# Optimization experiments

Hardware: AMD Instinct MI355X
Metric: run time of the kernel (lower is better)

Reference implementation:

```python
import jax, jax.numpy as jnp
import numpy as np

B, T, C = 16, 4096, 64  # batch, seq_len, n_embd == head_size


def setup_inputs() -> dict:
    key = jax.random.key(0)
    k1, k2, k3, k4 = jax.random.split(key, 4)
    x = jax.random.normal(k1, (B, T, C), dtype=jnp.float32)
    Wq = jax.random.normal(k2, (C, C), dtype=jnp.float32) * (C ** -0.5)
    Wk = jax.random.normal(k3, (C, C), dtype=jnp.float32) * (C ** -0.5)
    Wv = jax.random.normal(k4, (C, C), dtype=jnp.float32) * (C ** -0.5)
    return {"x": x, "Wq": Wq, "Wk": Wk, "Wv": Wv}


def reference(x, Wq, Wk, Wv):
    # Single-head causal self-attention (dropout rate = 0.0 in source -> identity).
    q = jnp.einsum('btc,cd->btd', x, Wq)  # [B,T,D]
    k = jnp.einsum('btc,cd->btd', x, Wk)  # [B,T,D]
    v = jnp.einsum('btc,cd->btd', x, Wv)  # [B,T,D]
    scale = q.shape[-1] ** -0.5
    wei = jnp.einsum('btd,bsd->bts', q, k) * scale  # [B,T,T] scores
    causal = jnp.tril(jnp.ones((T, T), dtype=bool))  # [T,T]
    wei = jnp.where(causal[None, :, :], wei, jnp.finfo(wei.dtype).min)
    wei = jax.nn.softmax(wei, axis=-1)
    out = jnp.einsum('bts,bsd->btd', wei, v)  # [B,T,D]
    return out
```

## Files before the change

kernel.cpp:

```cpp
#include <hip/hip_runtime.h>
#include <hip/hip_bf16.h>
#include <math.h>

#define BATCH 16
#define SEQ 4096
#define HDIM 64

typedef __attribute__((ext_vector_type(8))) short bf16x8;
typedef __attribute__((ext_vector_type(4))) float f32x4;
typedef __attribute__((ext_vector_type(4))) unsigned int u32x4;
typedef __attribute__((ext_vector_type(8))) unsigned short us8;

#define QSCALE 0.1803368801111601f

static __device__ __forceinline__ float exp2_fast(float x) {
#if __has_builtin(__builtin_amdgcn_exp2f)
    return __builtin_amdgcn_exp2f(x);
#else
    float r; asm("v_exp_f32 %0, %1" : "=v"(r) : "v"(x)); return r;
#endif
}

static __device__ __forceinline__ void load_lds16(const void* g, void* l) {
    __builtin_amdgcn_global_load_lds(
        (const __attribute__((address_space(1))) unsigned int*)g,
        (__attribute__((address_space(3))) unsigned int*)l,
        16, 0, 0);
}

static __device__ __forceinline__ unsigned short bf16bits(float f) {
    __hip_bfloat16 h = __float2bfloat16(f);
    return *(unsigned short*)&h;
}

static __device__ __forceinline__ unsigned int pack_bf16_trunc(float f0, float f1) {
    unsigned int u0 = __builtin_bit_cast(unsigned int, f0);
    unsigned int u1 = __builtin_bit_cast(unsigned int, f1);
#if __has_builtin(__builtin_amdgcn_perm)
    return __builtin_amdgcn_perm(u1, u0, 0x07060302u);
#else
    return (u1 & 0xFFFF0000u) | (u0 >> 16);
#endif
}

__global__ __launch_bounds__(256)
void wconv_kernel(const float* __restrict__ Wq,
                  const float* __restrict__ Wk,
                  const float* __restrict__ Wv,
                  __hip_bfloat16* __restrict__ wsw) {
    const int mat = blockIdx.x;
    const int tid = threadIdx.x;
    const float* W = (mat == 0) ? Wq : (mat == 1) ? Wk : Wv;
    const float sc = (mat == 0) ? QSCALE : 1.0f;
    #pragma unroll
    for (int c2 = 0; c2 < 2; ++c2) {
        const int chunk = c2 * 256 + tid;
        const int n = chunk & 63;
        const int c = chunk >> 6;
        us8 u;
        #pragma unroll
        for (int j = 0; j < 8; ++j)
            u[j] = bf16bits(W[(c * 8 + j) * HDIM + n] * sc);
        *(us8*)(wsw + mat * 4096 + n * 64 + (size_t)(c ^ (n & 7)) * 8) = u;
    }
}

__global__ __launch_bounds__(256)
void qkv_mfma_kernel(const float* __restrict__ x,
                     const __hip_bfloat16* __restrict__ wsw,
                     __hip_bfloat16* __restrict__ qb,
                     __hip_bfloat16* __restrict__ kb,
                     __hip_bfloat16* __restrict__ vt) {
    __shared__ __attribute__((aligned(16))) __hip_bfloat16 swt[3 * 64 * 64];
    __shared__ __attribute__((aligned(16))) char spool[16384];
    float* sx = (float*)spool;
    __hip_bfloat16 (*sout)[80] = (__hip_bfloat16 (*)[80])spool;

    const int tid = threadIdx.x;
    const int wv = tid >> 6;
    const int lane = tid & 63;
    const int quad = lane >> 4;
    const int ml = lane & 15;
    const size_t row0 = (size_t)blockIdx.x * 64;
    const int batch = (int)(row0 >> 12);
    const int t0 = (int)(row0 & 4095);

    #pragma unroll
    for (int r = 0; r < 6; ++r)
        load_lds16(wsw + (size_t)(r * 256 + tid) * 8, swt + (size_t)(r * 256 + tid) * 8);
    #pragma unroll
    for (int r = 0; r < 4; ++r)
        load_lds16(x + row0 * HDIM + (size_t)(r * 256 + tid) * 4, sx + (size_t)(r * 256 + tid) * 4);
    asm volatile("s_waitcnt vmcnt(0)" ::: "memory");
    __syncthreads();

    bf16x8 a0, a1;
    {
        const float* xr = sx + (size_t)(wv * 16 + ml) * HDIM + quad * 8;
        f32x4 lo = *(const f32x4*)xr;
        f32x4 hi = *(const f32x4*)(xr + 4);
        u32x4 pk;
        pk[0] = pack_bf16_trunc(lo[0], lo[1]);
        pk[1] = pack_bf16_trunc(lo[2], lo[3]);
        pk[2] = pack_bf16_trunc(hi[0], hi[1]);
        pk[3] = pack_bf16_trunc(hi[2], hi[3]);
        a0 = __builtin_bit_cast(bf16x8, pk);
        lo = *(const f32x4*)(xr + 32);
        hi = *(const f32x4*)(xr + 36);
        pk[0] = pack_bf16_trunc(lo[0], lo[1]);
        pk[1] = pack_bf16_trunc(lo[2], lo[3]);
        pk[2] = pack_bf16_trunc(hi[0], hi[1]);
        pk[3] = pack_bf16_trunc(hi[2], hi[3]);
        a1 = __builtin_bit_cast(bf16x8, pk);
    }
    __syncthreads();

    #pragma unroll
    for (int mat = 0; mat < 3; ++mat) {
        const __hip_bfloat16* wb = swt + mat * 4096;
        f32x4 acc[4];
        #pragma unroll
        for (int nt = 0; nt < 4; ++nt) {
            const int n = nt * 16 + ml;
            const int nx = n & 7;
            const bf16x8 bl = *(const bf16x8*)(wb + (size_t)n * 64 + (size_t)((quad) ^ nx) * 8);
            const bf16x8 bh = *(const bf16x8*)(wb + (size_t)n * 64 + (size_t)((quad + 4) ^ nx) * 8);
            acc[nt] = __builtin_amdgcn_mfma_f32_16x16x32_bf16(a0, bl, (f32x4){0.f,0.f,0.f,0.f}, 0, 0, 0);
            acc[nt] = __builtin_amdgcn_mfma_f32_16x16x32_bf16(a1, bh, acc[nt], 0, 0, 0);
        }

        if (mat < 2) {
            #pragma unroll
            for (int nt = 0; nt < 4; ++nt)
                #pragma unroll
                for (int r = 0; r < 4; ++r)
                    sout[wv * 16 + quad * 4 + r][nt * 16 + ml] = __float2bfloat16(acc[nt][r]);
        } else {
            #pragma unroll
            for (int nt = 0; nt < 4; ++nt)
                #pragma unroll
                for (int r = 0; r < 4; ++r)
                    sout[nt * 16 + ml][(wv >> 1) * 32 + quad * 8 + (wv & 1) * 4 + r] =
                        __float2bfloat16(acc[nt][r]);
        }
        __syncthreads();
        __hip_bfloat16* dst = (mat == 0) ? qb : (mat == 1) ? kb : vt;
        #pragma unroll
        for (int c2 = 0; c2 < 2; ++c2) {
            const int cc = c2 * 256 + tid;
            const int row = cc >> 3, g = cc & 7;
            us8 u = *(const us8*)&sout[row][g * 8];
            if (mat < 2)
                *(us8*)(dst + (row0 + row) * HDIM + g * 8) = u;
            else
                *(us8*)(dst + ((size_t)batch * HDIM + row) * SEQ + t0 + g * 8) = u;
        }
        __syncthreads();
    }
}

__global__ __launch_bounds__(256, 4)
void flash_mfma_kernel(const __hip_bfloat16* __restrict__ qb,
                       const __hip_bfloat16* __restrict__ kbuf,
                       const __hip_bfloat16* __restrict__ vt,
                       float* __restrict__ out) {
    __shared__ __attribute__((aligned(16))) __hip_bfloat16 smem[16384];

    const int tid = threadIdx.x;
    const int wv = tid >> 6;
    const int lane = tid & 63;
    const int quad = lane >> 4;
    const int ml = lane & 15;
    const int mh = wv & 1;
    const int kh = wv >> 1;

    const int id = blockIdx.x;
    const int b = id & 15;
    const int t = id >> 4;
    const int hi2 = t >> 4, mid = t & 15;
    const int qt = (hi2 == 0) ? (63 - mid)
                 : (hi2 == 1) ? (32 + mid)
                 : (hi2 == 2) ? (31 - mid) : mid;
    const int qbw = qt * 64 + mh * 32;
    const size_t bb = (size_t)b * SEQ * HDIM;

    const __hip_bfloat16* Q = qb + bb;
    const __hip_bfloat16* K = kbuf + bb;
    const __hip_bfloat16* VT = vt + bb;

    bf16x8 bq[2][2];
    #pragma unroll
    for (int qi = 0; qi < 2; ++qi)
        #pragma unroll
        for (int h = 0; h < 2; ++h)
            bq[qi][h] = *(const bf16x8*)(Q + (size_t)(qbw + qi * 16 + ml) * HDIM + h * 32 + quad * 8);

    bf16x8 ones8;
    #pragma unroll
    for (int j = 0; j < 8; ++j) ones8[j] = (short)0x3F80;

    f32x4 acc[4][2];
    #pragma unroll
    for (int nt = 0; nt < 4; ++nt)
        #pragma unroll
        for (int qi = 0; qi < 2; ++qi) acc[nt][qi] = (f32x4){0.f, 0.f, 0.f, 0.f};
    f32x4 lacc[2] = {(f32x4){0.f,0.f,0.f,0.f}, (f32x4){0.f,0.f,0.f,0.f}};

    const int s0 = wv * 128 + lane;
    const int s1 = s0 + 64;
    const int r0row = s0 >> 3, r0ch = (s0 & 7) ^ (r0row & 7);
    const int r1row = s1 >> 3, r1ch = (s1 & 7) ^ (r1row & 7);
    const int d0 = (wv * 128) * 8;
    const int d1 = (wv * 128 + 64) * 8;

    int koff[2][2], voff[4];
    #pragma unroll
    for (int kt = 0; kt < 2; ++kt) {
        const int row = kh * 32 + kt * 16 + ml;
        const int rb = row << 3, rxx = row & 7;
        koff[kt][0] = (rb | (quad ^ rxx)) * 8;
        koff[kt][1] = (rb | ((quad + 4) ^ rxx)) * 8;
    }
    #pragma unroll
    for (int nt = 0; nt < 4; ++nt) {
        const int row = nt * 16 + ml;
        const int rb = row << 3, rxx = row & 7;
        voff[nt] = (rb | ((kh * 4 + quad) ^ rxx)) * 8;
    }

    load_lds16(K + (size_t)r0row * HDIM + r0ch * 8, smem + d0);
    load_lds16(K + (size_t)r1row * HDIM + r1ch * 8, smem + d1);
    load_lds16(VT + (size_t)r0row * SEQ + r0ch * 8, smem + 8192 + d0);
    load_lds16(VT + (size_t)r1row * SEQ + r1ch * 8, smem + 8192 + d1);
    asm volatile("s_waitcnt vmcnt(0)" ::: "memory");
    __syncthreads();

    for (int tile = 0; tile < qt; ++tile) {
        const int sel = (tile & 1) * 4096;
        const int nsel = 4096 - sel;
        const __hip_bfloat16* sk = smem + sel;
        const __hip_bfloat16* sv = smem + 8192 + sel;

        const int nk = tile * 64 + 64;
        load_lds16(K + (size_t)(nk + r0row) * HDIM + r0ch * 8, smem + nsel + d0);
        load_lds16(K + (size_t)(nk + r1row) * HDIM + r1ch * 8, smem + nsel + d1);
        load_lds16(VT + (size_t)r0row * SEQ + nk + r0ch * 8, smem + 8192 + nsel + d0);
        load_lds16(VT + (size_t)r1row * SEQ + nk + r1ch * 8, smem + 8192 + nsel + d1);

        bf16x8 kf[2][2], va[4];
        #pragma unroll
        for (int kt = 0; kt < 2; ++kt) {
            kf[kt][0] = *(const bf16x8*)(sk + koff[kt][0]);
            kf[kt][1] = *(const bf16x8*)(sk + koff[kt][1]);
        }
        #pragma unroll
        for (int nt = 0; nt < 4; ++nt)
            va[nt] = *(const bf16x8*)(sv + voff[nt]);

        f32x4 st[2][2];
        __builtin_amdgcn_s_setprio(1);
        #pragma unroll
        for (int kt = 0; kt < 2; ++kt)
            #pragma unroll
            for (int qi = 0; qi < 2; ++qi) {
                st[kt][qi] = __builtin_amdgcn_mfma_f32_16x16x32_bf16(kf[kt][0], bq[qi][0], (f32x4){0.f,0.f,0.f,0.f}, 0, 0, 0);
                st[kt][qi] = __builtin_amdgcn_mfma_f32_16x16x32_bf16(kf[kt][1], bq[qi][1], st[kt][qi], 0, 0, 0);
            }
        __builtin_amdgcn_s_setprio(0);

        bf16x8 p80;
        {
            float pv[8];
            #pragma unroll
            for (int half = 0; half < 2; ++half)
                #pragma unroll
                for (int r = 0; r < 4; ++r)
                    pv[half * 4 + r] = exp2_fast(st[half][0][r]);
            u32x4 pk;
            #pragma unroll
            for (int d = 0; d < 4; ++d)
                pk[d] = pack_bf16_trunc(pv[2 * d], pv[2 * d + 1]);
            p80 = __builtin_bit_cast(bf16x8, pk);
        }

        __builtin_amdgcn_s_setprio(1);
        lacc[0] = __builtin_amdgcn_mfma_f32_16x16x32_bf16(ones8, p80, lacc[0], 0, 0, 0);
        #pragma unroll
        for (int nt = 0; nt < 4; ++nt)
            acc[nt][0] = __builtin_amdgcn_mfma_f32_16x16x32_bf16(va[nt], p80, acc[nt][0], 0, 0, 0);
        __builtin_amdgcn_s_setprio(0);

        bf16x8 p81;
        {
            float pv[8];
            #pragma unroll
            for (int half = 0; half < 2; ++half)
                #pragma unroll
                for (int r = 0; r < 4; ++r)
                    pv[half * 4 + r] = exp2_fast(st[half][1][r]);
            u32x4 pk;
            #pragma unroll
            for (int d = 0; d < 4; ++d)
                pk[d] = pack_bf16_trunc(pv[2 * d], pv[2 * d + 1]);
            p81 = __builtin_bit_cast(bf16x8, pk);
        }

        __builtin_amdgcn_s_setprio(1);
        lacc[1] = __builtin_amdgcn_mfma_f32_16x16x32_bf16(ones8, p81, lacc[1], 0, 0, 0);
        #pragma unroll
        for (int nt = 0; nt < 4; ++nt)
            acc[nt][1] = __builtin_amdgcn_mfma_f32_16x16x32_bf16(va[nt], p81, acc[nt][1], 0, 0, 0);
        __builtin_amdgcn_s_setprio(0);

        asm volatile("s_waitcnt vmcnt(0)" ::: "memory");
        __syncthreads();
    }

    {
        const int kb0 = qt * 64;
        const int sel = (qt & 1) * 4096;
        const __hip_bfloat16* sk = smem + sel;
        const __hip_bfloat16* sv = smem + 8192 + sel;

        if (!(kh == 1 && mh == 0)) {
            bf16x8 kf[2][2], va[4];
            #pragma unroll
            for (int kt = 0; kt < 2; ++kt) {
                kf[kt][0] = *(const bf16x8*)(sk + koff[kt][0]);
                kf[kt][1] = *(const bf16x8*)(sk + koff[kt][1]);
            }
            #pragma unroll
            for (int nt = 0; nt < 4; ++nt)
                va[nt] = *(const bf16x8*)(sv + voff[nt]);

            f32x4 st[2][2];
            #pragma unroll
            for (int kt = 0; kt < 2; ++kt)
                #pragma unroll
                for (int qi = 0; qi < 2; ++qi) {
                    st[kt][qi] = __builtin_amdgcn_mfma_f32_16x16x32_bf16(kf[kt][0], bq[qi][0], (f32x4){0.f,0.f,0.f,0.f}, 0, 0, 0);
                    st[kt][qi] = __builtin_amdgcn_mfma_f32_16x16x32_bf16(kf[kt][1], bq[qi][1], st[kt][qi], 0, 0, 0);
                }

            bf16x8 p8[2];
            #pragma unroll
            for (int qi = 0; qi < 2; ++qi) {
                const int q = qbw + qi * 16 + ml;
                float pv[8];
                #pragma unroll
                for (int half = 0; half < 2; ++half)
                    #pragma unroll
                    for (int r = 0; r < 4; ++r) {
                        const int key = kb0 + kh * 32 + half * 16 + quad * 4 + r;
                        float pval = exp2_fast(st[half][qi][r]);
                        if (key > q) pval = 0.f;
                        pv[half * 4 + r] = pval;
                    }
                u32x4 pk;
                #pragma unroll
                for (int d = 0; d < 4; ++d)
                    pk[d] = pack_bf16_trunc(pv[2 * d], pv[2 * d + 1]);
                p8[qi] = __builtin_bit_cast(bf16x8, pk);
            }

            lacc[0] = __builtin_amdgcn_mfma_f32_16x16x32_bf16(ones8, p8[0], lacc[0], 0, 0, 0);
            lacc[1] = __builtin_amdgcn_mfma_f32_16x16x32_bf16(ones8, p8[1], lacc[1], 0, 0, 0);
            #pragma unroll
            for (int nt = 0; nt < 4; ++nt) {
                acc[nt][0] = __builtin_amdgcn_mfma_f32_16x16x32_bf16(va[nt], p8[0], acc[nt][0], 0, 0, 0);
                acc[nt][1] = __builtin_amdgcn_mfma_f32_16x16x32_bf16(va[nt], p8[1], acc[nt][1], 0, 0, 0);
            }
        }
    }

    float (*smerge)[64][18] = (float (*)[64][18])smem;
    #pragma unroll
    for (int qi = 0; qi < 2; ++qi) {
        __syncthreads();
        if (kh == 1) {
            float* mrow = smerge[mh][lane];
            #pragma unroll
            for (int nt = 0; nt < 4; ++nt)
                #pragma unroll
                for (int r = 0; r < 4; ++r) mrow[nt * 4 + r] = acc[nt][qi][r];
            mrow[16] = lacc[qi][0];
        }
        __syncthreads();
        if (kh == 0) {
            const float* mrow = smerge[mh][lane];
            const float inv = 1.0f / (lacc[qi][0] + mrow[16]);
            float* orow = out + bb + (size_t)(qbw + qi * 16 + ml) * HDIM;
            #pragma unroll
            for (int nt = 0; nt < 4; ++nt) {
                float4 o;
                o.x = (acc[nt][qi][0] + mrow[nt * 4 + 0]) * inv;
                o.y = (acc[nt][qi][1] + mrow[nt * 4 + 1]) * inv;
                o.z = (acc[nt][qi][2] + mrow[nt * 4 + 2]) * inv;
                o.w = (acc[nt][qi][3] + mrow[nt * 4 + 3]) * inv;
                *(float4*)(orow + nt * 16 + quad * 4) = o;
            }
        }
    }
}

extern "C" void kernel_launch(void* const* d_in, const int* in_sizes, int n_in,
                              void* d_out, int out_size, void* d_ws, size_t ws_size,
                              hipStream_t stream) {
    const float* x  = (const float*)d_in[0];
    const float* Wq = (const float*)d_in[1];
    const float* Wk = (const float*)d_in[2];
    const float* Wv = (const float*)d_in[3];
    float* outp = (float*)d_out;

    const size_t elems = (size_t)BATCH * SEQ * HDIM;
    __hip_bfloat16* qb = (__hip_bfloat16*)d_ws;
    __hip_bfloat16* kb = qb + elems;
    __hip_bfloat16* vt = kb + elems;
    __hip_bfloat16* wsw = vt + elems;

    wconv_kernel<<<dim3(3), 256, 0, stream>>>(Wq, Wk, Wv, wsw);
    qkv_mfma_kernel<<<dim3(BATCH * SEQ / 64), 256, 0, stream>>>(x, wsw, qb, kb, vt);
    flash_mfma_kernel<<<dim3(BATCH * SEQ / 64), 256, 0, stream>>>(qb, kb, vt, outp);
}
```

Baseline: 118.7 us.

## Split flash attention work across eight waves with one query subtile each

The flash attention kernel now launches 512 threads per block. Each wave owns a single 16-row query subtile instead of two, which halves per-wave accumulator registers and doubles waves per block. K/V tile loads are spread over eight waves at one load each, and the final cross-key-half merge runs once instead of per subtile. The QKV projection also swaps its packed truncation for a per-element bf16 conversion, which may change rounding and instruction count. The cost is more waves sharing each LDS tile, duplicated K/V fragment reads per wave, and higher barrier cost.

```diff
diff --git a/kernel.cpp b/kernel.cpp
--- a/kernel.cpp
+++ b/kernel.cpp
@@ -97,21 +97,10 @@
     bf16x8 a0, a1;
     {
         const float* xr = sx + (size_t)(wv * 16 + ml) * HDIM + quad * 8;
-        f32x4 lo = *(const f32x4*)xr;
-        f32x4 hi = *(const f32x4*)(xr + 4);
-        u32x4 pk;
-        pk[0] = pack_bf16_trunc(lo[0], lo[1]);
-        pk[1] = pack_bf16_trunc(lo[2], lo[3]);
-        pk[2] = pack_bf16_trunc(hi[0], hi[1]);
-        pk[3] = pack_bf16_trunc(hi[2], hi[3]);
-        a0 = __builtin_bit_cast(bf16x8, pk);
-        lo = *(const f32x4*)(xr + 32);
-        hi = *(const f32x4*)(xr + 36);
-        pk[0] = pack_bf16_trunc(lo[0], lo[1]);
-        pk[1] = pack_bf16_trunc(lo[2], lo[3]);
-        pk[2] = pack_bf16_trunc(hi[0], hi[1]);
-        pk[3] = pack_bf16_trunc(hi[2], hi[3]);
-        a1 = __builtin_bit_cast(bf16x8, pk);
+        #pragma unroll
+        for (int j = 0; j < 8; ++j) a0[j] = (short)bf16bits(xr[j]);
+        #pragma unroll
+        for (int j = 0; j < 8; ++j) a1[j] = (short)bf16bits(xr[32 + j]);
     }
     __syncthreads();
 
@@ -159,7 +148,7 @@
     }
 }
 
-__global__ __launch_bounds__(256, 4)
+__global__ __launch_bounds__(512, 8)
 void flash_mfma_kernel(const __hip_bfloat16* __restrict__ qb,
                        const __hip_bfloat16* __restrict__ kbuf,
                        const __hip_bfloat16* __restrict__ vt,
@@ -171,8 +160,9 @@
     const int lane = tid & 63;
     const int quad = lane >> 4;
     const int ml = lane & 15;
-    const int mh = wv & 1;
-    const int kh = wv >> 1;
+    const int kh = wv >> 2;
+    const int mh = (wv >> 1) & 1;
+    const int qj = wv & 1;
 
     const int id = blockIdx.x;
     const int b = id & 15;
@@ -181,37 +171,31 @@
     const int qt = (hi2 == 0) ? (63 - mid)
                  : (hi2 == 1) ? (32 + mid)
                  : (hi2 == 2) ? (31 - mid) : mid;
-    const int qbw = qt * 64 + mh * 32;
+    const int qbase = qt * 64 + mh * 32 + qj * 16;
     const size_t bb = (size_t)b * SEQ * HDIM;
 
     const __hip_bfloat16* Q = qb + bb;
     const __hip_bfloat16* K = kbuf + bb;
     const __hip_bfloat16* VT = vt + bb;
 
-    bf16x8 bq[2][2];
-    #pragma unroll
-    for (int qi = 0; qi < 2; ++qi)
-        #pragma unroll
-        for (int h = 0; h < 2; ++h)
-            bq[qi][h] = *(const bf16x8*)(Q + (size_t)(qbw + qi * 16 + ml) * HDIM + h * 32 + quad * 8);
+    bf16x8 bq[2];
+    #pragma unroll
+    for (int h = 0; h < 2; ++h)
+        bq[h] = *(const bf16x8*)(Q + (size_t)(qbase + ml) * HDIM + h * 32 + quad * 8);
 
     bf16x8 ones8;
     #pragma unroll
     for (int j = 0; j < 8; ++j) ones8[j] = (short)0x3F80;
 
-    f32x4 acc[4][2];
-    #pragma unroll
-    for (int nt = 0; nt < 4; ++nt)
-        #pragma unroll
-        for (int qi = 0; qi < 2; ++qi) acc[nt][qi] = (f32x4){0.f, 0.f, 0.f, 0.f};
-    f32x4 lacc[2] = {(f32x4){0.f,0.f,0.f,0.f}, (f32x4){0.f,0.f,0.f,0.f}};
-
-    const int s0 = wv * 128 + lane;
-    const int s1 = s0 + 64;
-    const int r0row = s0 >> 3, r0ch = (s0 & 7) ^ (r0row & 7);
-    const int r1row = s1 >> 3, r1ch = (s1 & 7) ^ (r1row & 7);
-    const int d0 = (wv * 128) * 8;
-    const int d1 = (wv * 128 + 64) * 8;
+    f32x4 acc[4];
+    #pragma unroll
+    for (int nt = 0; nt < 4; ++nt) acc[nt] = (f32x4){0.f, 0.f, 0.f, 0.f};
+    f32x4 lacc = (f32x4){0.f, 0.f, 0.f, 0.f};
+
+    const int kr = tid >> 3;
+    const int kc = (tid & 7) ^ (kr & 7);
+    __hip_bfloat16* const kds = smem + wv * 512;
+    __hip_bfloat16* const vds = smem + 8192 + wv * 512;
 
     int koff[2][2], voff[4];
     #pragma unroll
@@ -228,10 +212,8 @@
         voff[nt] = (rb | ((kh * 4 + quad) ^ rxx)) * 8;
     }
 
-    load_lds16(K + (size_t)r0row * HDIM + r0ch * 8, smem + d0);
-    load_lds16(K + (size_t)r1row * HDIM + r1ch * 8, smem + d1);
-    load_lds16(VT + (size_t)r0row * SEQ + r0ch * 8, smem + 8192 + d0);
-    load_lds16(VT + (size_t)r1row * SEQ + r1ch * 8, smem + 8192 + d1);
+    load_lds16(K + (size_t)kr * HDIM + kc * 8, kds);
+    load_lds16(VT + (size_t)kr * SEQ + kc * 8, vds);
     asm volatile("s_waitcnt vmcnt(0)" ::: "memory");
     __syncthreads();
 
@@ -242,74 +224,50 @@
         const __hip_bfloat16* sv = smem + 8192 + sel;
 
         const int nk = tile * 64 + 64;
-        load_lds16(K + (size_t)(nk + r0row) * HDIM + r0ch * 8, smem + nsel + d0);
-        load_lds16(K + (size_t)(nk + r1row) * HDIM + r1ch * 8, smem + nsel + d1);
-        load_lds16(VT + (size_t)r0row * SEQ + nk + r0ch * 8, smem + 8192 + nsel + d0);
-        load_lds16(VT + (size_t)r1row * SEQ + nk + r1ch * 8, smem + 8192 + nsel + d1);
-
-        bf16x8 kf[2][2], va[4];
+        load_lds16(K + (size_t)(nk + kr) * HDIM + kc * 8, smem + nsel + wv * 512);
+        load_lds16(VT + (size_t)kr * SEQ + nk + kc * 8, smem + 8192 + nsel + wv * 512);
+
+        bf16x8 kf[2][2];
         #pragma unroll
         for (int kt = 0; kt < 2; ++kt) {
             kf[kt][0] = *(const bf16x8*)(sk + koff[kt][0]);
             kf[kt][1] = *(const bf16x8*)(sk + koff[kt][1]);
         }
+
+        f32x4 st[2];
+        __builtin_amdgcn_s_setprio(1);
+        #pragma unroll
+        for (int kt = 0; kt < 2; ++kt) {
+            st[kt] = __builtin_amdgcn_mfma_f32_16x16x32_bf16(kf[kt][0], bq[0], (f32x4){0.f,0.f,0.f,0.f}, 0, 0, 0);
+            st[kt] = __builtin_amdgcn_mfma_f32_16x16x32_bf16(kf[kt][1], bq[1], st[kt], 0, 0, 0);
+        }
+        __builtin_amdgcn_s_setprio(0);
+
+        bf16x8 va[4];
         #pragma unroll
         for (int nt = 0; nt < 4; ++nt)
             va[nt] = *(const bf16x8*)(sv + voff[nt]);
 
-        f32x4 st[2][2];
-        __builtin_amdgcn_s_setprio(1);
-        #pragma unroll
-        for (int kt = 0; kt < 2; ++kt)
-            #pragma unroll
-            for (int qi = 0; qi < 2; ++qi) {
-                st[kt][qi] = __builtin_amdgcn_mfma_f32_16x16x32_bf16(kf[kt][0], bq[qi][0], (f32x4){0.f,0.f,0.f,0.f}, 0, 0, 0);
-                st[kt][qi] = __builtin_amdgcn_mfma_f32_16x16x32_bf16(kf[kt][1], bq[qi][1], st[kt][qi], 0, 0, 0);
-            }
-        __builtin_amdgcn_s_setprio(0);
-
-        bf16x8 p80;
+        bf16x8 p8;
         {
             float pv[8];
             #pragma unroll
-            for (int half = 0; half < 2; ++half)
+            for (int kt = 0; kt < 2; ++kt)
                 #pragma unroll
                 for (int r = 0; r < 4; ++r)
-                    pv[half * 4 + r] = exp2_fast(st[half][0][r]);
+                    pv[kt * 4 + r] = exp2_fast(st[kt][r]);
             u32x4 pk;
             #pragma unroll
             for (int d = 0; d < 4; ++d)
                 pk[d] = pack_bf16_trunc(pv[2 * d], pv[2 * d + 1]);
-            p80 = __builtin_bit_cast(bf16x8, pk);
+            p8 = __builtin_bit_cast(bf16x8, pk);
         }
 
         __builtin_amdgcn_s_setprio(1);
-        lacc[0] = __builtin_amdgcn_mfma_f32_16x16x32_bf16(ones8, p80, lacc[0], 0, 0, 0);
+        lacc = __builtin_amdgcn_mfma_f32_16x16x32_bf16(ones8, p8, lacc, 0, 0, 0);
         #pragma unroll
         for (int nt = 0; nt < 4; ++nt)
-            acc[nt][0] = __builtin_amdgcn_mfma_f32_16x16x32_bf16(va[nt], p80, acc[nt][0], 0, 0, 0);
-        __builtin_amdgcn_s_setprio(0);
-
-        bf16x8 p81;
-        {
-            float pv[8];
-            #pragma unroll
-            for (int half = 0; half < 2; ++half)
-                #pragma unroll
-                for (int r = 0; r < 4; ++r)
-                    pv[half * 4 + r] = exp2_fast(st[half][1][r]);
-            u32x4 pk;
-            #pragma unroll
-            for (int d = 0; d < 4; ++d)
-                pk[d] = pack_bf16_trunc(pv[2 * d], pv[2 * d + 1]);
-            p81 = __builtin_bit_cast(bf16x8, pk);
-        }
-
-        __builtin_amdgcn_s_setprio(1);
-        lacc[1] = __builtin_amdgcn_mfma_f32_16x16x32_bf16(ones8, p81, lacc[1], 0, 0, 0);
-        #pragma unroll
-        for (int nt = 0; nt < 4; ++nt)
-            acc[nt][1] = __builtin_amdgcn_mfma_f32_16x16x32_bf16(va[nt], p81, acc[nt][1], 0, 0, 0);
+            acc[nt] = __builtin_amdgcn_mfma_f32_16x16x32_bf16(va[nt], p8, acc[nt], 0, 0, 0);
         __builtin_amdgcn_s_setprio(0);
 
         asm volatile("s_waitcnt vmcnt(0)" ::: "memory");
@@ -323,82 +281,74 @@
         const __hip_bfloat16* sv = smem + 8192 + sel;
 
         if (!(kh == 1 && mh == 0)) {
-            bf16x8 kf[2][2], va[4];
+            bf16x8 kf[2][2];
             #pragma unroll
             for (int kt = 0; kt < 2; ++kt) {
                 kf[kt][0] = *(const bf16x8*)(sk + koff[kt][0]);
                 kf[kt][1] = *(const bf16x8*)(sk + koff[kt][1]);
             }
+            f32x4 st[2];
+            #pragma unroll
+            for (int kt = 0; kt < 2; ++kt) {
+                st[kt] = __builtin_amdgcn_mfma_f32_16x16x32_bf16(kf[kt][0], bq[0], (f32x4){0.f,0.f,0.f,0.f}, 0, 0, 0);
+                st[kt] = __builtin_amdgcn_mfma_f32_16x16x32_bf16(kf[kt][1], bq[1], st[kt], 0, 0, 0);
+            }
+            bf16x8 va[4];
             #pragma unroll
             for (int nt = 0; nt < 4; ++nt)
                 va[nt] = *(const bf16x8*)(sv + voff[nt]);
 
-            f32x4 st[2][2];
-            #pragma unroll
-            for (int kt = 0; kt < 2; ++kt)
-                #pragma unroll
-                for (int qi = 0; qi < 2; ++qi) {
-                    st[kt][qi] = __builtin_amdgcn_mfma_f32_16x16x32_bf16(kf[kt][0], bq[qi][0], (f32x4){0.f,0.f,0.f,0.f}, 0, 0, 0);
-                    st[kt][qi] = __builtin_amdgcn_mfma_f32_16x16x32_bf16(kf[kt][1], bq[qi][1], st[kt][qi], 0, 0, 0);
-                }
-
-            bf16x8 p8[2];
-            #pragma unroll
-            for (int qi = 0; qi < 2; ++qi) {
-                const int q = qbw + qi * 16 + ml;
+            bf16x8 p8;
+            {
+                const int q = qbase + ml;
                 float pv[8];
                 #pragma unroll
-                for (int half = 0; half < 2; ++half)
+                for (int kt = 0; kt < 2; ++kt)
                     #pragma unroll
                     for (int r = 0; r < 4; ++r) {
-                        const int key = kb0 + kh * 32 + half * 16 + quad * 4 + r;
-                        float pval = exp2_fast(st[half][qi][r]);
+                        const int key = kb0 + kh * 32 + kt * 16 + quad * 4 + r;
+                        float pval = exp2_fast(st[kt][r]);
                         if (key > q) pval = 0.f;
-                        pv[half * 4 + r] = pval;
+                        pv[kt * 4 + r] = pval;
                     }
                 u32x4 pk;
                 #pragma unroll
                 for (int d = 0; d < 4; ++d)
                     pk[d] = pack_bf16_trunc(pv[2 * d], pv[2 * d + 1]);
-                p8[qi] = __builtin_bit_cast(bf16x8, pk);
+                p8 = __builtin_bit_cast(bf16x8, pk);
             }
 
-            lacc[0] = __builtin_amdgcn_mfma_f32_16x16x32_bf16(ones8, p8[0], lacc[0], 0, 0, 0);
-            lacc[1] = __builtin_amdgcn_mfma_f32_16x16x32_bf16(ones8, p8[1], lacc[1], 0, 0, 0);
-            #pragma unroll
-            for (int nt = 0; nt < 4; ++nt) {
-                acc[nt][0] = __builtin_amdgcn_mfma_f32_16x16x32_bf16(va[nt], p8[0], acc[nt][0], 0, 0, 0);
-                acc[nt][1] = __builtin_amdgcn_mfma_f32_16x16x32_bf16(va[nt], p8[1], acc[nt][1], 0, 0, 0);
-            }
+            lacc = __builtin_amdgcn_mfma_f32_16x16x32_bf16(ones8, p8, lacc, 0, 0, 0);
+            #pragma unroll
+            for (int nt = 0; nt < 4; ++nt)
+                acc[nt] = __builtin_amdgcn_mfma_f32_16x16x32_bf16(va[nt], p8, acc[nt], 0, 0, 0);
         }
     }
 
     float (*smerge)[64][18] = (float (*)[64][18])smem;
-    #pragma unroll
-    for (int qi = 0; qi < 2; ++qi) {
-        __syncthreads();
-        if (kh == 1) {
-            float* mrow = smerge[mh][lane];
-            #pragma unroll
-            for (int nt = 0; nt < 4; ++nt)
-                #pragma unroll
-                for (int r = 0; r < 4; ++r) mrow[nt * 4 + r] = acc[nt][qi][r];
-            mrow[16] = lacc[qi][0];
-        }
-        __syncthreads();
-        if (kh == 0) {
-            const float* mrow = smerge[mh][lane];
-            const float inv = 1.0f / (lacc[qi][0] + mrow[16]);
-            float* orow = out + bb + (size_t)(qbw + qi * 16 + ml) * HDIM;
-            #pragma unroll
-            for (int nt = 0; nt < 4; ++nt) {
-                float4 o;
-                o.x = (acc[nt][qi][0] + mrow[nt * 4 + 0]) * inv;
-                o.y = (acc[nt][qi][1] + mrow[nt * 4 + 1]) * inv;
-                o.z = (acc[nt][qi][2] + mrow[nt * 4 + 2]) * inv;
-                o.w = (acc[nt][qi][3] + mrow[nt * 4 + 3]) * inv;
-                *(float4*)(orow + nt * 16 + quad * 4) = o;
-            }
+    const int pid = wv & 3;
+    __syncthreads();
+    if (kh == 1) {
+        float* mrow = smerge[pid][lane];
+        #pragma unroll
+        for (int nt = 0; nt < 4; ++nt)
+            #pragma unroll
+            for (int r = 0; r < 4; ++r) mrow[nt * 4 + r] = acc[nt][r];
+        mrow[16] = lacc[0];
+    }
+    __syncthreads();
+    if (kh == 0) {
+        const float* mrow = smerge[pid][lane];
+        const float inv = 1.0f / (lacc[0] + mrow[16]);
+        float* orow = out + bb + (size_t)(qbase + ml) * HDIM;
+        #pragma unroll
+        for (int nt = 0; nt < 4; ++nt) {
+            float4 o;
+            o.x = (acc[nt][0] + mrow[nt * 4 + 0]) * inv;
+            o.y = (acc[nt][1] + mrow[nt * 4 + 1]) * inv;
+            o.z = (acc[nt][2] + mrow[nt * 4 + 2]) * inv;
+            o.w = (acc[nt][3] + mrow[nt * 4 + 3]) * inv;
+            *(float4*)(orow + nt * 16 + quad * 4) = o;
         }
     }
 }
@@ -420,5 +370,5 @@
 
     wconv_kernel<<<dim3(3), 256, 0, stream>>>(Wq, Wk, Wv, wsw);
     qkv_mfma_kernel<<<dim3(BATCH * SEQ / 64), 256, 0, stream>>>(x, wsw, qb, kb, vt);
-    flash_mfma_kernel<<<dim3(BATCH * SEQ / 64), 256, 0, stream>>>(qb, kb, vt, outp);
-}
+    flash_mfma_kernel<<<dim3(BATCH * SEQ / 64), 512, 0, stream>>>(qb, kb, vt, outp);
+}
```

New measurement: 209.3 us. 76.4% more time.

## Triple-buffer K tiles to prefetch two tiles ahead in flash kernel

Applied to the files above, without the earlier changes.

The flash attention kernel now keeps three K buffers and two V buffers in LDS, raising shared memory from 32KB to 40KB. K is prefetched two tiles ahead and V one tile ahead. The end-of-tile wait becomes vmcnt(2), so the K load for tile+2 can stay in flight across the barrier. The projection kernel's bf16 conversion of x is also rewritten as a per-element loop. The extra LDS may lower occupancy, and the waitcnt accounting depends on load ordering.

```diff
diff --git a/kernel.cpp b/kernel.cpp
--- a/kernel.cpp
+++ b/kernel.cpp
@@ -97,21 +97,10 @@
     bf16x8 a0, a1;
     {
         const float* xr = sx + (size_t)(wv * 16 + ml) * HDIM + quad * 8;
-        f32x4 lo = *(const f32x4*)xr;
-        f32x4 hi = *(const f32x4*)(xr + 4);
-        u32x4 pk;
-        pk[0] = pack_bf16_trunc(lo[0], lo[1]);
-        pk[1] = pack_bf16_trunc(lo[2], lo[3]);
-        pk[2] = pack_bf16_trunc(hi[0], hi[1]);
-        pk[3] = pack_bf16_trunc(hi[2], hi[3]);
-        a0 = __builtin_bit_cast(bf16x8, pk);
-        lo = *(const f32x4*)(xr + 32);
-        hi = *(const f32x4*)(xr + 36);
-        pk[0] = pack_bf16_trunc(lo[0], lo[1]);
-        pk[1] = pack_bf16_trunc(lo[2], lo[3]);
-        pk[2] = pack_bf16_trunc(hi[0], hi[1]);
-        pk[3] = pack_bf16_trunc(hi[2], hi[3]);
-        a1 = __builtin_bit_cast(bf16x8, pk);
+        #pragma unroll
+        for (int j = 0; j < 8; ++j) a0[j] = (short)bf16bits(xr[j]);
+        #pragma unroll
+        for (int j = 0; j < 8; ++j) a1[j] = (short)bf16bits(xr[32 + j]);
     }
     __syncthreads();
 
@@ -164,7 +153,7 @@
                        const __hip_bfloat16* __restrict__ kbuf,
                        const __hip_bfloat16* __restrict__ vt,
                        float* __restrict__ out) {
-    __shared__ __attribute__((aligned(16))) __hip_bfloat16 smem[16384];
+    __shared__ __attribute__((aligned(16))) __hip_bfloat16 smem[20480];
 
     const int tid = threadIdx.x;
     const int wv = tid >> 6;
@@ -230,22 +219,33 @@
 
     load_lds16(K + (size_t)r0row * HDIM + r0ch * 8, smem + d0);
     load_lds16(K + (size_t)r1row * HDIM + r1ch * 8, smem + d1);
-    load_lds16(VT + (size_t)r0row * SEQ + r0ch * 8, smem + 8192 + d0);
-    load_lds16(VT + (size_t)r1row * SEQ + r1ch * 8, smem + 8192 + d1);
-    asm volatile("s_waitcnt vmcnt(0)" ::: "memory");
+    load_lds16(VT + (size_t)r0row * SEQ + r0ch * 8, smem + 12288 + d0);
+    load_lds16(VT + (size_t)r1row * SEQ + r1ch * 8, smem + 12288 + d1);
+    if (qt >= 1) {
+        load_lds16(K + (size_t)(64 + r0row) * HDIM + r0ch * 8, smem + 4096 + d0);
+        load_lds16(K + (size_t)(64 + r1row) * HDIM + r1ch * 8, smem + 4096 + d1);
+        asm volatile("s_waitcnt vmcnt(2)" ::: "memory");
+    } else {
+        asm volatile("s_waitcnt vmcnt(0)" ::: "memory");
+    }
     __syncthreads();
 
+    int curk = 0;
     for (int tile = 0; tile < qt; ++tile) {
-        const int sel = (tile & 1) * 4096;
-        const int nsel = 4096 - sel;
-        const __hip_bfloat16* sk = smem + sel;
-        const __hip_bfloat16* sv = smem + 8192 + sel;
-
-        const int nk = tile * 64 + 64;
-        load_lds16(K + (size_t)(nk + r0row) * HDIM + r0ch * 8, smem + nsel + d0);
-        load_lds16(K + (size_t)(nk + r1row) * HDIM + r1ch * 8, smem + nsel + d1);
-        load_lds16(VT + (size_t)r0row * SEQ + nk + r0ch * 8, smem + 8192 + nsel + d0);
-        load_lds16(VT + (size_t)r1row * SEQ + nk + r1ch * 8, smem + 8192 + nsel + d1);
+        const __hip_bfloat16* sk = smem + curk * 4096;
+        const __hip_bfloat16* sv = smem + 12288 + (tile & 1) * 4096;
+
+        const int nv = tile * 64 + 64;
+        const int vdst = 12288 + ((tile + 1) & 1) * 4096;
+        load_lds16(VT + (size_t)r0row * SEQ + nv + r0ch * 8, smem + vdst + d0);
+        load_lds16(VT + (size_t)r1row * SEQ + nv + r1ch * 8, smem + vdst + d1);
+        const bool havek2 = (tile + 2 <= qt);
+        if (havek2) {
+            const int nk = tile * 64 + 128;
+            const int k2 = (curk >= 1) ? (curk - 1) : 2;
+            load_lds16(K + (size_t)(nk + r0row) * HDIM + r0ch * 8, smem + k2 * 4096 + d0);
+            load_lds16(K + (size_t)(nk + r1row) * HDIM + r1ch * 8, smem + k2 * 4096 + d1);
+        }
 
         bf16x8 kf[2][2], va[4];
         #pragma unroll
@@ -312,15 +312,16 @@
             acc[nt][1] = __builtin_amdgcn_mfma_f32_16x16x32_bf16(va[nt], p81, acc[nt][1], 0, 0, 0);
         __builtin_amdgcn_s_setprio(0);
 
-        asm volatile("s_waitcnt vmcnt(0)" ::: "memory");
+        if (havek2) asm volatile("s_waitcnt vmcnt(2)" ::: "memory");
+        else        asm volatile("s_waitcnt vmcnt(0)" ::: "memory");
         __syncthreads();
+        curk = (curk == 2) ? 0 : curk + 1;
     }
 
     {
         const int kb0 = qt * 64;
-        const int sel = (qt & 1) * 4096;
-        const __hip_bfloat16* sk = smem + sel;
-        const __hip_bfloat16* sv = smem + 8192 + sel;
+        const __hip_bfloat16* sk = smem + curk * 4096;
+        const __hip_bfloat16* sv = smem + 12288 + (qt & 1) * 4096;
 
         if (!(kh == 1 && mh == 0)) {
             bf16x8 kf[2][2], va[4];
```

New measurement: 124.5 us. 4.9% more time.

## Use 128-query blocks with 8 waves sharing K/V tiles in flash kernel

Applied to the files above, without the earlier changes.

The flash kernel now processes 128 query rows per block with 512 threads (two 64-row query halves), so each K/V tile loaded into LDS is reused by twice as many waves. This halves the global loads per query and the block count. The block-to-work mapping pairs short and long causal ranges, and an extra diagonal tile is handled for the upper half. The QKV kernel's x-to-bf16 conversion is rewritten as a per-element loop. Risks include lower occupancy from the larger blocks and the extra tail-tile work.

```diff
diff --git a/kernel.cpp b/kernel.cpp
--- a/kernel.cpp
+++ b/kernel.cpp
@@ -97,21 +97,10 @@
     bf16x8 a0, a1;
     {
         const float* xr = sx + (size_t)(wv * 16 + ml) * HDIM + quad * 8;
-        f32x4 lo = *(const f32x4*)xr;
-        f32x4 hi = *(const f32x4*)(xr + 4);
-        u32x4 pk;
-        pk[0] = pack_bf16_trunc(lo[0], lo[1]);
-        pk[1] = pack_bf16_trunc(lo[2], lo[3]);
-        pk[2] = pack_bf16_trunc(hi[0], hi[1]);
-        pk[3] = pack_bf16_trunc(hi[2], hi[3]);
-        a0 = __builtin_bit_cast(bf16x8, pk);
-        lo = *(const f32x4*)(xr + 32);
-        hi = *(const f32x4*)(xr + 36);
-        pk[0] = pack_bf16_trunc(lo[0], lo[1]);
-        pk[1] = pack_bf16_trunc(lo[2], lo[3]);
-        pk[2] = pack_bf16_trunc(hi[0], hi[1]);
-        pk[3] = pack_bf16_trunc(hi[2], hi[3]);
-        a1 = __builtin_bit_cast(bf16x8, pk);
+        #pragma unroll
+        for (int j = 0; j < 8; ++j) a0[j] = (short)bf16bits(xr[j]);
+        #pragma unroll
+        for (int j = 0; j < 8; ++j) a1[j] = (short)bf16bits(xr[32 + j]);
     }
     __syncthreads();
 
@@ -159,7 +148,7 @@
     }
 }
 
-__global__ __launch_bounds__(256, 4)
+__global__ __launch_bounds__(512, 4)
 void flash_mfma_kernel(const __hip_bfloat16* __restrict__ qb,
                        const __hip_bfloat16* __restrict__ kbuf,
                        const __hip_bfloat16* __restrict__ vt,
@@ -171,17 +160,15 @@
     const int lane = tid & 63;
     const int quad = lane >> 4;
     const int ml = lane & 15;
-    const int mh = wv & 1;
-    const int kh = wv >> 1;
+    const int qh = wv >> 2;
+    const int mh = (wv >> 1) & 1;
+    const int kh = wv & 1;
 
     const int id = blockIdx.x;
     const int b = id & 15;
-    const int t = id >> 4;
-    const int hi2 = t >> 4, mid = t & 15;
-    const int qt = (hi2 == 0) ? (63 - mid)
-                 : (hi2 == 1) ? (32 + mid)
-                 : (hi2 == 2) ? (31 - mid) : mid;
-    const int qbw = qt * 64 + mh * 32;
+    const int pp = id >> 4;
+    const int p = (pp < 16) ? pp : 47 - pp;
+    const int qbw = p * 128 + qh * 64 + mh * 32;
     const size_t bb = (size_t)b * SEQ * HDIM;
 
     const __hip_bfloat16* Q = qb + bb;
@@ -206,12 +193,9 @@
         for (int qi = 0; qi < 2; ++qi) acc[nt][qi] = (f32x4){0.f, 0.f, 0.f, 0.f};
     f32x4 lacc[2] = {(f32x4){0.f,0.f,0.f,0.f}, (f32x4){0.f,0.f,0.f,0.f}};
 
-    const int s0 = wv * 128 + lane;
-    const int s1 = s0 + 64;
-    const int r0row = s0 >> 3, r0ch = (s0 & 7) ^ (r0row & 7);
-    const int r1row = s1 >> 3, r1ch = (s1 & 7) ^ (r1row & 7);
-    const int d0 = (wv * 128) * 8;
-    const int d1 = (wv * 128 + 64) * 8;
+    const int kr = tid >> 3;
+    const int kc = (tid & 7) ^ (kr & 7);
+    const int dstoff = wv * 512;
 
     int koff[2][2], voff[4];
     #pragma unroll
@@ -228,24 +212,21 @@
         voff[nt] = (rb | ((kh * 4 + quad) ^ rxx)) * 8;
     }
 
-    load_lds16(K + (size_t)r0row * HDIM + r0ch * 8, smem + d0);
-    load_lds16(K + (size_t)r1row * HDIM + r1ch * 8, smem + d1);
-    load_lds16(VT + (size_t)r0row * SEQ + r0ch * 8, smem + 8192 + d0);
-    load_lds16(VT + (size_t)r1row * SEQ + r1ch * 8, smem + 8192 + d1);
+    load_lds16(K + (size_t)kr * HDIM + kc * 8, smem + dstoff);
+    load_lds16(VT + (size_t)kr * SEQ + kc * 8, smem + 8192 + dstoff);
     asm volatile("s_waitcnt vmcnt(0)" ::: "memory");
     __syncthreads();
 
-    for (int tile = 0; tile < qt; ++tile) {
+    const int nfull = 2 * p;
+    for (int tile = 0; tile < nfull; ++tile) {
         const int sel = (tile & 1) * 4096;
         const int nsel = 4096 - sel;
         const __hip_bfloat16* sk = smem + sel;
         const __hip_bfloat16* sv = smem + 8192 + sel;
 
         const int nk = tile * 64 + 64;
-        load_lds16(K + (size_t)(nk + r0row) * HDIM + r0ch * 8, smem + nsel + d0);
-        load_lds16(K + (size_t)(nk + r1row) * HDIM + r1ch * 8, smem + nsel + d1);
-        load_lds16(VT + (size_t)r0row * SEQ + nk + r0ch * 8, smem + 8192 + nsel + d0);
-        load_lds16(VT + (size_t)r1row * SEQ + nk + r1ch * 8, smem + 8192 + nsel + d1);
+        load_lds16(K + (size_t)(nk + kr) * HDIM + kc * 8, smem + nsel + dstoff);
+        load_lds16(VT + (size_t)kr * SEQ + nk + kc * 8, smem + 8192 + nsel + dstoff);
 
         bf16x8 kf[2][2], va[4];
         #pragma unroll
@@ -317,12 +298,15 @@
     }
 
     {
-        const int kb0 = qt * 64;
-        const int sel = (qt & 1) * 4096;
-        const __hip_bfloat16* sk = smem + sel;
-        const __hip_bfloat16* sv = smem + 8192 + sel;
-
-        if (!(kh == 1 && mh == 0)) {
+        const int kb0 = nfull * 64;
+        const __hip_bfloat16* sk = smem;
+        const __hip_bfloat16* sv = smem + 8192;
+
+        const int nk = kb0 + 64;
+        load_lds16(K + (size_t)(nk + kr) * HDIM + kc * 8, smem + 4096 + dstoff);
+        load_lds16(VT + (size_t)kr * SEQ + nk + kc * 8, smem + 12288 + dstoff);
+
+        if (!(qh == 0 && kh == 1 && mh == 0)) {
             bf16x8 kf[2][2], va[4];
             #pragma unroll
             for (int kt = 0; kt < 2; ++kt) {
@@ -371,14 +355,73 @@
                 acc[nt][1] = __builtin_amdgcn_mfma_f32_16x16x32_bf16(va[nt], p8[1], acc[nt][1], 0, 0, 0);
             }
         }
+        asm volatile("s_waitcnt vmcnt(0)" ::: "memory");
+        __syncthreads();
+    }
+
+    {
+        const int kb0 = nfull * 64 + 64;
+        const __hip_bfloat16* sk = smem + 4096;
+        const __hip_bfloat16* sv = smem + 12288;
+
+        if (qh == 1 && !(kh == 1 && mh == 0)) {
+            bf16x8 kf[2][2], va[4];
+            #pragma unroll
+            for (int kt = 0; kt < 2; ++kt) {
+                kf[kt][0] = *(const bf16x8*)(sk + koff[kt][0]);
+                kf[kt][1] = *(const bf16x8*)(sk + koff[kt][1]);
+            }
+            #pragma unroll
+            for (int nt = 0; nt < 4; ++nt)
+                va[nt] = *(const bf16x8*)(sv + voff[nt]);
+
+            f32x4 st[2][2];
+            #pragma unroll
+            for (int kt = 0; kt < 2; ++kt)
+                #pragma unroll
+                for (int qi = 0; qi < 2; ++qi) {
+                    st[kt][qi] = __builtin_amdgcn_mfma_f32_16x16x32_bf16(kf[kt][0], bq[qi][0], (f32x4){0.f,0.f,0.f,0.f}, 0, 0, 0);
+                    st[kt][qi] = __builtin_amdgcn_mfma_f32_16x16x32_bf16(kf[kt][1], bq[qi][1], st[kt][qi], 0, 0, 0);
+                }
+
+            bf16x8 p8[2];
+            #pragma unroll
+            for (int qi = 0; qi < 2; ++qi) {
+                const int q = qbw + qi * 16 + ml;
+                float pv[8];
+                #pragma unroll
+                for (int half = 0; half < 2; ++half)
+                    #pragma unroll
+                    for (int r = 0; r < 4; ++r) {
+                        const int key = kb0 + kh * 32 + half * 16 + quad * 4 + r;
+                        float pval = exp2_fast(st[half][qi][r]);
+                        if (key > q) pval = 0.f;
+                        pv[half * 4 + r] = pval;
+                    }
+                u32x4 pk;
+                #pragma unroll
+                for (int d = 0; d < 4; ++d)
+                    pk[d] = pack_bf16_trunc(pv[2 * d], pv[2 * d + 1]);
+                p8[qi] = __builtin_bit_cast(bf16x8, pk);
+            }
+
+            lacc[0] = __builtin_amdgcn_mfma_f32_16x16x32_bf16(ones8, p8[0], lacc[0], 0, 0, 0);
+            lacc[1] = __builtin_amdgcn_mfma_f32_16x16x32_bf16(ones8, p8[1], lacc[1], 0, 0, 0);
+            #pragma unroll
+            for (int nt = 0; nt < 4; ++nt) {
+                acc[nt][0] = __builtin_amdgcn_mfma_f32_16x16x32_bf16(va[nt], p8[0], acc[nt][0], 0, 0, 0);
+                acc[nt][1] = __builtin_amdgcn_mfma_f32_16x16x32_bf16(va[nt], p8[1], acc[nt][1], 0, 0, 0);
+            }
+        }
     }
 
     float (*smerge)[64][18] = (float (*)[64][18])smem;
+    const int pid = wv >> 1;
     #pragma unroll
     for (int qi = 0; qi < 2; ++qi) {
         __syncthreads();
         if (kh == 1) {
-            float* mrow = smerge[mh][lane];
+            float* mrow = smerge[pid][lane];
             #pragma unroll
             for (int nt = 0; nt < 4; ++nt)
                 #pragma unroll
@@ -387,7 +430,7 @@
         }
         __syncthreads();
         if (kh == 0) {
-            const float* mrow = smerge[mh][lane];
+            const float* mrow = smerge[pid][lane];
             const float inv = 1.0f / (lacc[qi][0] + mrow[16]);
             float* orow = out + bb + (size_t)(qbw + qi * 16 + ml) * HDIM;
             #pragma unroll
@@ -420,5 +463,5 @@
 
     wconv_kernel<<<dim3(3), 256, 0, stream>>>(Wq, Wk, Wv, wsw);
     qkv_mfma_kernel<<<dim3(BATCH * SEQ / 64), 256, 0, stream>>>(x, wsw, qb, kb, vt);
-    flash_mfma_kernel<<<dim3(BATCH * SEQ / 64), 256, 0, stream>>>(qb, kb, vt, outp);
-}
+    flash_mfma_kernel<<<dim3(BATCH * SEQ / 128), 512, 0, stream>>>(qb, kb, vt, outp);
+}
```

Result: slower. 121.6 us (+2.4%).
